# Performance work log

Measured on AMD Instinct MI355X. Metric: run time of the kernel, lower is better.

## Reference

```python
import jax, jax.numpy as jnp
import numpy as np

BEAM_SIZE = 16


def setup_inputs() -> dict:
    key = jax.random.key(0)
    ks = jax.random.split(key, 9)
    B, N, S, A, Ai, E = 4, 48, 32, 16, 8, 512
    unaries = jax.random.normal(ks[0], (B, N, S), jnp.float32)
    behaviors = jax.random.normal(ks[1], (B, N, S, A), jnp.float32)
    interactions = jax.random.normal(ks[2], (B, N, N, S, S, Ai), jnp.float32)
    masks = jnp.ones((B, N), jnp.bool_)
    behavior_masks = jax.random.bernoulli(ks[3], 0.5, (S, A))
    interaction_masks = jax.random.bernoulli(ks[4], 0.5, (S, S, Ai))
    binary_edges = jax.random.randint(ks[5], (B, E, 2), 0, N, jnp.int32)
    binary_masks = jnp.ones((B, E), jnp.bool_)
    targets = jax.random.randint(ks[6], (B, N), 0, S, jnp.int32)
    weight_param_unary = jax.random.uniform(ks[7], (S,), jnp.float32)
    weight_param_binary = jax.random.uniform(ks[8], (S, S), jnp.float32)
    return dict(unaries=unaries, behaviors=behaviors, interactions=interactions,
                weight_param_unary=weight_param_unary, weight_param_binary=weight_param_binary,
                masks=masks, behavior_masks=behavior_masks, interaction_masks=interaction_masks,
                binary_edges=binary_edges, binary_masks=binary_masks, targets=targets)


def _forward(unaries, behaviors, interactions, weight_param_unary, weight_param_binary,
             masks, behavior_masks, interaction_masks, binary_edges, binary_masks, targets):
    sg = jax.lax.stop_gradient  # mirrors torch.no_grad blocks
    B, N, S = unaries.shape
    E = binary_edges.shape[1]
    K = min(BEAM_SIZE, S)
    dt = unaries.dtype

    m = masks[..., None].astype(dt)                                  # (B,N,1)
    masked_unaries = sg(unaries * m)                                 # no_grad
    bmask = behavior_masks.astype(dt)                                # (S,A)
    acnt = bmask.sum(-1)
    acnt = jnp.where(acnt == 0, jnp.ones((), dt), acnt)              # (S,)
    behaviors_unaries = sg(((behaviors * bmask).sum(-1) / acnt) * m) # (B,N,S), no_grad

    weighted_unaries = masked_unaries + weight_param_unary * behaviors_unaries

    # --- beam selection (targets forced to beam slot 0 via +inf scatter) ---
    bi = jnp.arange(B)[:, None]
    ni = jnp.arange(N)[None, :]
    _u = weighted_unaries.at[bi, ni, targets].set(jnp.inf)
    beam_targets = jax.lax.top_k(sg(_u), K)[1]                       # (B,N,K) int
    beam_unary = jnp.take_along_axis(weighted_unaries, beam_targets, axis=2)  # (B,N,K)

    # --- binary potentials: masked mean over interaction actions ---
    imask = interaction_masks.astype(dt)                             # (S,S,Ai)
    icnt = imask.sum(-1)
    icnt = jnp.where(icnt == 0, jnp.ones((), dt), icnt)              # (S,S)
    masked_inter = (interactions * imask).sum(-1) / icnt             # (B,N,N,S,S)

    eb = jnp.arange(B)[:, None]
    sel = masked_inter[eb, binary_edges[..., 0], binary_edges[..., 1]]  # (B,E,S,S)
    bt1 = beam_targets[eb, binary_edges[..., 0]]                     # (B,E,K)
    bt2 = beam_targets[eb, binary_edges[..., 1]]                     # (B,E,K)
    bin_phis_init = sg(sel[jnp.arange(B)[:, None, None, None],
                           jnp.arange(E)[None, :, None, None],
                           bt1[:, :, :, None], bt2[:, :, None, :]])  # (B,E,K,K), no_grad
    bin_phis = bin_phis_init * weight_param_binary[bt1[:, :, :, None], bt2[:, :, None, :]]

    # --- piecewise pseudo-likelihood loss ---
    norm_unary = jax.nn.log_softmax(beam_unary, axis=-1)
    gold_unary = jnp.where(masks, norm_unary[:, :, 0], jnp.zeros((), dt))
    pll = gold_unary.sum(-1)                                         # (B,)
    norm_bin = jax.nn.log_softmax(bin_phis.reshape(B, E, K * K), axis=-1).reshape(B, E, K, K)
    gold_bin = jnp.where(binary_masks, norm_bin[:, :, 0, 0], jnp.zeros((), dt))
    pll = pll + gold_bin.sum(-1)
    nll = -(pll / masks.sum(-1).astype(dt)).mean()
    return nll


def reference(unaries, behaviors, interactions, weight_param_unary, weight_param_binary,
              masks, behavior_masks, interaction_masks, binary_edges, binary_masks, targets):
    return _forward(unaries, behaviors, interactions, weight_param_unary, weight_param_binary,
                    masks, behavior_masks, interaction_masks, binary_edges, binary_masks, targets)
```

## Files before the change

kernel.cpp:

```cpp
#include <hip/hip_runtime.h>
#include <hip/hip_bf16.h>
#include <math.h>

#define BB 4
#define NN 48
#define SS 32
#define AA 16
#define AI 8
#define EE 512
#define KK 16
#define NNODE (BB * NN)
#define NEDGE (BB * EE)

#define WS_NG    0
#define WS_EG    1024

__device__ __forceinline__ bool read_mask(const void* p, int idx, int flag) {
    if (flag == 1) return ((const unsigned char*)p)[idx] != 0;
    if (flag == 2) return ((const float*)p)[idx] != 0.0f;
    return ((const int*)p)[idx] != 0;
}

__device__ __forceinline__ int detect_flag(const void* bmask, int lane) {
    unsigned int wrd = ((const unsigned int*)bmask)[lane & 31];
    bool anyF = __any(wrd == 0x3F800000u);
    bool anyG = __any(wrd > 1u);
    return anyF ? 2 : (anyG ? 1 : 0);
}

__device__ __forceinline__ void node_beam(
    int node, int lane, int flag,
    const float* __restrict__ unaries, const float* __restrict__ behaviors,
    const void* masks, const int* __restrict__ targets,
    const float* __restrict__ wpu, const void* bmask,
    int* beam16, float* gold_out)
{
    float m = read_mask(masks, node, flag) ? 1.f : 0.f;
    int tgt = targets[node];

    float val = -INFINITY, key = -INFINITY;
    if (lane < SS) {
        int s = lane;
        float u = unaries[node * SS + s];

        const float4* bp4 = (const float4*)(behaviors + ((size_t)node * SS + s) * AA);
        float4 b0 = bp4[0], b1 = bp4[1], b2 = bp4[2], b3 = bp4[3];
        float bv[16] = {b0.x,b0.y,b0.z,b0.w, b1.x,b1.y,b1.z,b1.w,
                        b2.x,b2.y,b2.z,b2.w, b3.x,b3.y,b3.z,b3.w};

        float bmv[16];
        if (flag == 1) {
            uint4 v = *(const uint4*)((const unsigned char*)bmask + s * 16);
            unsigned int w4[4] = {v.x, v.y, v.z, v.w};
            #pragma unroll
            for (int k = 0; k < 16; ++k)
                bmv[k] = ((w4[k >> 2] >> ((k & 3) * 8)) & 255u) ? 1.f : 0.f;
        } else if (flag == 0) {
            const uint4* ip = (const uint4*)((const int*)bmask + s * 16);
            #pragma unroll
            for (int r = 0; r < 4; ++r) {
                uint4 v = ip[r];
                bmv[r*4+0] = v.x ? 1.f : 0.f; bmv[r*4+1] = v.y ? 1.f : 0.f;
                bmv[r*4+2] = v.z ? 1.f : 0.f; bmv[r*4+3] = v.w ? 1.f : 0.f;
            }
        } else {
            const float4* fp = (const float4*)((const float*)bmask + s * 16);
            #pragma unroll
            for (int r = 0; r < 4; ++r) {
                float4 v = fp[r];
                bmv[r*4+0] = v.x != 0.f ? 1.f : 0.f; bmv[r*4+1] = v.y != 0.f ? 1.f : 0.f;
                bmv[r*4+2] = v.z != 0.f ? 1.f : 0.f; bmv[r*4+3] = v.w != 0.f ? 1.f : 0.f;
            }
        }

        float cnt = 0.f, raw = 0.f;
        #pragma unroll
        for (int k = 0; k < 16; ++k) { cnt += bmv[k]; raw += bmv[k] * bv[k]; }
        if (cnt == 0.f) cnt = 1.f;
        val = m * (u + wpu[s] * (raw / cnt));
        key = (s == tgt) ? INFINITY : val;
    }

    int rank = 0;
    #pragma unroll
    for (int t = 0; t < SS; ++t) {
        float kt = __shfl(key, t, 64);
        rank += (kt > key) || (kt == key && t < lane);
    }
    bool sel = (lane < SS) && (rank < KK);

    if (beam16) {
        bool sel_nt = sel && (lane != tgt);
        unsigned long long bal = __ballot(sel_nt);
        if (sel) {
            int slot = (lane == tgt) ? 0
                       : 1 + __popcll(bal & ((1ull << lane) - 1ull));
            beam16[slot] = lane;
        }
    }

    if (gold_out) {
        float mv = sel ? val : -INFINITY;
        #pragma unroll
        for (int off = 32; off >= 1; off >>= 1)
            mv = fmaxf(mv, __shfl_xor(mv, off, 64));
        float se = sel ? expf(val - mv) : 0.f;
        #pragma unroll
        for (int off = 32; off >= 1; off >>= 1)
            se += __shfl_xor(se, off, 64);
        float vt = __shfl(val, tgt, 64);
        if (lane == 0)
            *gold_out = (m > 0.f) ? (vt - mv - logf(se)) : 0.f;
    }
}

__global__ __launch_bounds__(256) void main_kernel(
    const float* __restrict__ unaries,
    const float* __restrict__ behaviors,
    const float* __restrict__ interactions,
    const float* __restrict__ wpu,
    const float* __restrict__ wpb,
    const void* masks, const void* bmask, const void* imask,
    const int* __restrict__ edges, const void* binmask,
    const int* __restrict__ targets,
    float* __restrict__ node_gold,
    float* __restrict__ edge_gold)
{
    int be = blockIdx.x;
    int b = be >> 9;
    int tid = threadIdx.x;
    int wid = tid >> 6, lane = tid & 63;
    int flag = detect_flag(bmask, lane);

    int2 e2 = ((const int2*)edges)[be];
    int n1 = e2.x, n2 = e2.y;

    __shared__ int beamA[KK], beamB[KK];

    bool active = (wid < 2) || (wid == 2 && be < NNODE);
    if (active) {
        int node = (wid == 0) ? (b * NN + n1)
                 : (wid == 1) ? (b * NN + n2) : be;
        int* bptr = (wid == 0) ? beamA : (wid == 1) ? beamB : nullptr;
        float* gptr = (wid == 2) ? &node_gold[be] : nullptr;
        node_beam(node, lane, flag, unaries, behaviors, masks, targets,
                  wpu, bmask, bptr, gptr);
    }
    __syncthreads();

    int i = tid >> 4, j = tid & 15;
    int s1 = beamA[i], s2 = beamB[j];
    int p = s1 * SS + s2;

    size_t base = (((size_t)(b * NN + n1) * NN + n2) * (SS * SS) + p) * AI;
    float4 x0 = *(const float4*)(interactions + base);
    float4 x1 = *(const float4*)(interactions + base + 4);
    float xv[8] = {x0.x,x0.y,x0.z,x0.w, x1.x,x1.y,x1.z,x1.w};

    float imv[8];
    if (flag == 1) {
        uint2 v = *(const uint2*)((const unsigned char*)imask + p * 8);
        unsigned int w2[2] = {v.x, v.y};
        #pragma unroll
        for (int k = 0; k < 8; ++k)
            imv[k] = ((w2[k >> 2] >> ((k & 3) * 8)) & 255u) ? 1.f : 0.f;
    } else if (flag == 0) {
        const uint4* ip = (const uint4*)((const int*)imask + p * 8);
        uint4 v0 = ip[0], v1 = ip[1];
        imv[0]=v0.x?1.f:0.f; imv[1]=v0.y?1.f:0.f; imv[2]=v0.z?1.f:0.f; imv[3]=v0.w?1.f:0.f;
        imv[4]=v1.x?1.f:0.f; imv[5]=v1.y?1.f:0.f; imv[6]=v1.z?1.f:0.f; imv[7]=v1.w?1.f:0.f;
    } else {
        const float4* fp = (const float4*)((const float*)imask + p * 8);
        float4 v0 = fp[0], v1 = fp[1];
        imv[0]=v0.x!=0.f?1.f:0.f; imv[1]=v0.y!=0.f?1.f:0.f; imv[2]=v0.z!=0.f?1.f:0.f; imv[3]=v0.w!=0.f?1.f:0.f;
        imv[4]=v1.x!=0.f?1.f:0.f; imv[5]=v1.y!=0.f?1.f:0.f; imv[6]=v1.z!=0.f?1.f:0.f; imv[7]=v1.w!=0.f?1.f:0.f;
    }
    float cnt = 0.f, raw = 0.f;
    #pragma unroll
    for (int k = 0; k < 8; ++k) { cnt += imv[k]; raw += imv[k] * xv[k]; }
    if (cnt == 0.f) cnt = 1.f;
    float phi = wpb[p] * (raw / cnt);

    float mw = phi;
    #pragma unroll
    for (int off = 32; off >= 1; off >>= 1)
        mw = fmaxf(mw, __shfl_xor(mw, off, 64));
    float ew = expf(phi - mw);
    #pragma unroll
    for (int off = 32; off >= 1; off >>= 1)
        ew += __shfl_xor(ew, off, 64);

    __shared__ float2 sred[4];
    if (lane == 0) sred[wid] = make_float2(mw, ew);
    __syncthreads();

    if (tid == 0) {
        float2 p0 = sred[0], p1 = sred[1], p2 = sred[2], p3 = sred[3];
        float M = fmaxf(fmaxf(p0.x, p1.x), fmaxf(p2.x, p3.x));
        float S = p0.y * expf(p0.x - M) + p1.y * expf(p1.x - M)
                + p2.y * expf(p2.x - M) + p3.y * expf(p3.x - M);
        float gold = phi - M - logf(S);
        bool bm = read_mask(binmask, be, flag);
        edge_gold[be] = bm ? gold : 0.f;
    }
}

__global__ __launch_bounds__(256) void final_kernel(
    const void* masks, const void* bmask,
    const float* __restrict__ node_gold,
    const float* __restrict__ edge_gold,
    float* __restrict__ out)
{
    int tid = threadIdx.x;
    int b = tid >> 6;
    int lane = tid & 63;
    int flag = detect_flag(bmask, lane);

    float sum = 0.f, cnt = 0.f;
    if (lane < NN) {
        sum += node_gold[b * NN + lane];
        cnt += read_mask(masks, b * NN + lane, flag) ? 1.f : 0.f;
    }
    for (int e = lane; e < EE; e += 64)
        sum += edge_gold[b * EE + e];

    #pragma unroll
    for (int off = 32; off >= 1; off >>= 1) {
        sum += __shfl_xor(sum, off, 64);
        cnt += __shfl_xor(cnt, off, 64);
    }
    __shared__ float sp[4];
    if (lane == 0) sp[b] = sum / cnt;
    __syncthreads();
    if (tid == 0)
        out[0] = -(sp[0] + sp[1] + sp[2] + sp[3]) * (1.f / BB);
}

extern "C" void kernel_launch(void* const* d_in, const int* in_sizes, int n_in,
                              void* d_out, int out_size, void* d_ws, size_t ws_size,
                              hipStream_t stream) {
    const float* unaries      = (const float*)d_in[0];
    const float* behaviors    = (const float*)d_in[1];
    const float* interactions = (const float*)d_in[2];
    const float* wpu          = (const float*)d_in[3];
    const float* wpb          = (const float*)d_in[4];
    const void*  masks        = d_in[5];
    const void*  bmask        = d_in[6];
    const void*  imask        = d_in[7];
    const int*   edges        = (const int*)d_in[8];
    const void*  binmask      = d_in[9];
    const int*   targets      = (const int*)d_in[10];
    float* out = (float*)d_out;

    char* ws = (char*)d_ws;
    float* node_gold = (float*)(ws + WS_NG);
    float* edge_gold = (float*)(ws + WS_EG);

    main_kernel<<<NEDGE, 256, 0, stream>>>(unaries, behaviors, interactions,
                                           wpu, wpb, masks, bmask, imask,
                                           edges, binmask, targets,
                                           node_gold, edge_gold);
    final_kernel<<<1, 256, 0, stream>>>(masks, bmask, node_gold, edge_gold, out);
}
```

Measured before the change: 17.59 us.

## Compute per-wave redundant beams to drop block barrier; split node gold to extra blocks

Every wave now computes both endpoint beams itself, with each 32-lane half handling one node and writing to a per-wave shared slot. This removes the block-wide barrier between beam selection and the interaction pass. Node gold-unary work moves into 48 extra blocks, so edge blocks no longer carry a third divergent wave. The cost is fourfold redundant beam computation per edge block, paid to avoid the __syncthreads stall. The final reduction also reads edge_gold with float4 loads.

```diff
diff --git a/kernel.cpp b/kernel.cpp
--- a/kernel.cpp
+++ b/kernel.cpp
@@ -28,90 +28,48 @@
     return anyF ? 2 : (anyG ? 1 : 0);
 }
 
-__device__ __forceinline__ void node_beam(
-    int node, int lane, int flag,
+__device__ __forceinline__ float weighted_unary(
+    int node, int s, int flag, float m,
     const float* __restrict__ unaries, const float* __restrict__ behaviors,
-    const void* masks, const int* __restrict__ targets,
-    const float* __restrict__ wpu, const void* bmask,
-    int* beam16, float* gold_out)
+    const float* __restrict__ wpu, const void* bmask)
 {
-    float m = read_mask(masks, node, flag) ? 1.f : 0.f;
-    int tgt = targets[node];
-
-    float val = -INFINITY, key = -INFINITY;
-    if (lane < SS) {
-        int s = lane;
-        float u = unaries[node * SS + s];
-
-        const float4* bp4 = (const float4*)(behaviors + ((size_t)node * SS + s) * AA);
-        float4 b0 = bp4[0], b1 = bp4[1], b2 = bp4[2], b3 = bp4[3];
-        float bv[16] = {b0.x,b0.y,b0.z,b0.w, b1.x,b1.y,b1.z,b1.w,
-                        b2.x,b2.y,b2.z,b2.w, b3.x,b3.y,b3.z,b3.w};
-
-        float bmv[16];
-        if (flag == 1) {
-            uint4 v = *(const uint4*)((const unsigned char*)bmask + s * 16);
-            unsigned int w4[4] = {v.x, v.y, v.z, v.w};
-            #pragma unroll
-            for (int k = 0; k < 16; ++k)
-                bmv[k] = ((w4[k >> 2] >> ((k & 3) * 8)) & 255u) ? 1.f : 0.f;
-        } else if (flag == 0) {
-            const uint4* ip = (const uint4*)((const int*)bmask + s * 16);
-            #pragma unroll
-            for (int r = 0; r < 4; ++r) {
-                uint4 v = ip[r];
-                bmv[r*4+0] = v.x ? 1.f : 0.f; bmv[r*4+1] = v.y ? 1.f : 0.f;
-                bmv[r*4+2] = v.z ? 1.f : 0.f; bmv[r*4+3] = v.w ? 1.f : 0.f;
-            }
-        } else {
-            const float4* fp = (const float4*)((const float*)bmask + s * 16);
-            #pragma unroll
-            for (int r = 0; r < 4; ++r) {
-                float4 v = fp[r];
-                bmv[r*4+0] = v.x != 0.f ? 1.f : 0.f; bmv[r*4+1] = v.y != 0.f ? 1.f : 0.f;
-                bmv[r*4+2] = v.z != 0.f ? 1.f : 0.f; bmv[r*4+3] = v.w != 0.f ? 1.f : 0.f;
-            }
-        }
-
-        float cnt = 0.f, raw = 0.f;
-        #pragma unroll
-        for (int k = 0; k < 16; ++k) { cnt += bmv[k]; raw += bmv[k] * bv[k]; }
-        if (cnt == 0.f) cnt = 1.f;
-        val = m * (u + wpu[s] * (raw / cnt));
-        key = (s == tgt) ? INFINITY : val;
-    }
-
-    int rank = 0;
-    #pragma unroll
-    for (int t = 0; t < SS; ++t) {
-        float kt = __shfl(key, t, 64);
-        rank += (kt > key) || (kt == key && t < lane);
-    }
-    bool sel = (lane < SS) && (rank < KK);
-
-    if (beam16) {
-        bool sel_nt = sel && (lane != tgt);
-        unsigned long long bal = __ballot(sel_nt);
-        if (sel) {
-            int slot = (lane == tgt) ? 0
-                       : 1 + __popcll(bal & ((1ull << lane) - 1ull));
-            beam16[slot] = lane;
-        }
-    }
-
-    if (gold_out) {
-        float mv = sel ? val : -INFINITY;
-        #pragma unroll
-        for (int off = 32; off >= 1; off >>= 1)
-            mv = fmaxf(mv, __shfl_xor(mv, off, 64));
-        float se = sel ? expf(val - mv) : 0.f;
-        #pragma unroll
-        for (int off = 32; off >= 1; off >>= 1)
-            se += __shfl_xor(se, off, 64);
-        float vt = __shfl(val, tgt, 64);
-        if (lane == 0)
-            *gold_out = (m > 0.f) ? (vt - mv - logf(se)) : 0.f;
-    }
+    float u = unaries[node * SS + s];
+
+    const float4* bp4 = (const float4*)(behaviors + ((size_t)node * SS + s) * AA);
+    float4 b0 = bp4[0], b1 = bp4[1], b2 = bp4[2], b3 = bp4[3];
+    float bv[16] = {b0.x,b0.y,b0.z,b0.w, b1.x,b1.y,b1.z,b1.w,
+                    b2.x,b2.y,b2.z,b2.w, b3.x,b3.y,b3.z,b3.w};
+
+    float bmv[16];
+    if (flag == 1) {
+        uint4 v = *(const uint4*)((const unsigned char*)bmask + s * 16);
+        unsigned int w4[4] = {v.x, v.y, v.z, v.w};
+        #pragma unroll
+        for (int k = 0; k < 16; ++k)
+            bmv[k] = ((w4[k >> 2] >> ((k & 3) * 8)) & 255u) ? 1.f : 0.f;
+    } else if (flag == 0) {
+        const uint4* ip = (const uint4*)((const int*)bmask + s * 16);
+        #pragma unroll
+        for (int r = 0; r < 4; ++r) {
+            uint4 v = ip[r];
+            bmv[r*4+0] = v.x ? 1.f : 0.f; bmv[r*4+1] = v.y ? 1.f : 0.f;
+            bmv[r*4+2] = v.z ? 1.f : 0.f; bmv[r*4+3] = v.w ? 1.f : 0.f;
+        }
+    } else {
+        const float4* fp = (const float4*)((const float*)bmask + s * 16);
+        #pragma unroll
+        for (int r = 0; r < 4; ++r) {
+            float4 v = fp[r];
+            bmv[r*4+0] = v.x != 0.f ? 1.f : 0.f; bmv[r*4+1] = v.y != 0.f ? 1.f : 0.f;
+            bmv[r*4+2] = v.z != 0.f ? 1.f : 0.f; bmv[r*4+3] = v.w != 0.f ? 1.f : 0.f;
+        }
+    }
+
+    float cnt = 0.f, raw = 0.f;
+    #pragma unroll
+    for (int k = 0; k < 16; ++k) { cnt += bmv[k]; raw += bmv[k] * bv[k]; }
+    if (cnt == 0.f) cnt = 1.f;
+    return m * (u + wpu[s] * (raw / cnt));
 }
 
 __global__ __launch_bounds__(256) void main_kernel(
@@ -126,35 +84,85 @@
     float* __restrict__ node_gold,
     float* __restrict__ edge_gold)
 {
-    int be = blockIdx.x;
-    int b = be >> 9;
     int tid = threadIdx.x;
     int wid = tid >> 6, lane = tid & 63;
     int flag = detect_flag(bmask, lane);
 
+    if (blockIdx.x >= NEDGE) {
+        int node = (blockIdx.x - NEDGE) * 4 + wid;
+        float m = read_mask(masks, node, flag) ? 1.f : 0.f;
+        int tgt = targets[node];
+
+        float val = -INFINITY, key = -INFINITY;
+        if (lane < SS) {
+            val = weighted_unary(node, lane, flag, m, unaries, behaviors, wpu, bmask);
+            key = (lane == tgt) ? INFINITY : val;
+        }
+        int rank = 0;
+        #pragma unroll
+        for (int t = 0; t < SS; ++t) {
+            float kt = __shfl(key, t, 64);
+            rank += (kt > key) || (kt == key && t < lane);
+        }
+        bool sel = (lane < SS) && (rank < KK);
+
+        float mv = sel ? val : -INFINITY;
+        #pragma unroll
+        for (int off = 32; off >= 1; off >>= 1)
+            mv = fmaxf(mv, __shfl_xor(mv, off, 64));
+        float se = sel ? expf(val - mv) : 0.f;
+        #pragma unroll
+        for (int off = 32; off >= 1; off >>= 1)
+            se += __shfl_xor(se, off, 64);
+        float vt = __shfl(val, tgt, 64);
+        if (lane == 0)
+            node_gold[node] = (m > 0.f) ? (vt - mv - logf(se)) : 0.f;
+        return;
+    }
+
+    int be = blockIdx.x;
+    int b = be >> 9;
+    int half = lane >> 5;
+    int s = lane & 31;
+
     int2 e2 = ((const int2*)edges)[be];
     int n1 = e2.x, n2 = e2.y;
-
-    __shared__ int beamA[KK], beamB[KK];
-
-    bool active = (wid < 2) || (wid == 2 && be < NNODE);
-    if (active) {
-        int node = (wid == 0) ? (b * NN + n1)
-                 : (wid == 1) ? (b * NN + n2) : be;
-        int* bptr = (wid == 0) ? beamA : (wid == 1) ? beamB : nullptr;
-        float* gptr = (wid == 2) ? &node_gold[be] : nullptr;
-        node_beam(node, lane, flag, unaries, behaviors, masks, targets,
-                  wpu, bmask, bptr, gptr);
-    }
-    __syncthreads();
-
-    int i = tid >> 4, j = tid & 15;
-    int s1 = beamA[i], s2 = beamB[j];
+    int node = b * NN + (half ? n2 : n1);
+
+    __shared__ int beamW[4][2 * KK];
+    __shared__ float2 sred[4];
+
+    float m = read_mask(masks, node, flag) ? 1.f : 0.f;
+    int tgt = targets[node];
+    float val = weighted_unary(node, s, flag, m, unaries, behaviors, wpu, bmask);
+    float key = (s == tgt) ? INFINITY : val;
+
+    int base = half << 5;
+    int rank = 0;
+    #pragma unroll
+    for (int t = 0; t < SS; ++t) {
+        float kt = __shfl(key, base + t, 64);
+        rank += (kt > key) || (kt == key && t < s);
+    }
+    bool sel = rank < KK;
+
+    bool sel_nt = sel && (s != tgt);
+    unsigned long long bal = __ballot(sel_nt);
+    unsigned int hb = (unsigned int)(bal >> (half << 5));
+    if (sel) {
+        int slot = (s == tgt) ? 0 : 1 + __popc(hb & ((1u << s) - 1u));
+        beamW[wid][(half << 4) + slot] = s;
+    }
+
+    int i = (wid << 2) + (lane >> 4);
+    int j = lane & 15;
+    int s1 = beamW[wid][i];
+    int s2 = beamW[wid][16 + j];
     int p = s1 * SS + s2;
 
-    size_t base = (((size_t)(b * NN + n1) * NN + n2) * (SS * SS) + p) * AI;
-    float4 x0 = *(const float4*)(interactions + base);
-    float4 x1 = *(const float4*)(interactions + base + 4);
+    size_t gbase = (((size_t)(b * NN + n1) * NN + n2) * (SS * SS) + p) * AI;
+    float4 x0 = *(const float4*)(interactions + gbase);
+    float4 x1 = *(const float4*)(interactions + gbase + 4);
     float xv[8] = {x0.x,x0.y,x0.z,x0.w, x1.x,x1.y,x1.z,x1.w};
 
     float imv[8];
@@ -190,7 +198,6 @@
     for (int off = 32; off >= 1; off >>= 1)
         ew += __shfl_xor(ew, off, 64);
 
-    __shared__ float2 sred[4];
     if (lane == 0) sred[wid] = make_float2(mw, ew);
     __syncthreads();
 
@@ -221,8 +228,12 @@
         sum += node_gold[b * NN + lane];
         cnt += read_mask(masks, b * NN + lane, flag) ? 1.f : 0.f;
     }
-    for (int e = lane; e < EE; e += 64)
-        sum += edge_gold[b * EE + e];
+    const float4* eg4 = (const float4*)(edge_gold + b * EE);
+    #pragma unroll
+    for (int k = 0; k < 2; ++k) {
+        float4 v = eg4[(lane << 1) + k];
+        sum += v.x + v.y + v.z + v.w;
+    }
 
     #pragma unroll
     for (int off = 32; off >= 1; off >>= 1) {
@@ -256,9 +267,9 @@
     float* node_gold = (float*)(ws + WS_NG);
     float* edge_gold = (float*)(ws + WS_EG);
 
-    main_kernel<<<NEDGE, 256, 0, stream>>>(unaries, behaviors, interactions,
-                                           wpu, wpb, masks, bmask, imask,
-                                           edges, binmask, targets,
-                                           node_gold, edge_gold);
+    main_kernel<<<NEDGE + 48, 256, 0, stream>>>(unaries, behaviors, interactions,
+                                                wpu, wpb, masks, bmask, imask,
+                                                edges, binmask, targets,
+                                                node_gold, edge_gold);
     final_kernel<<<1, 256, 0, stream>>>(masks, bmask, node_gold, edge_gold, out);
 }
```

Result: no change. 17.65 us (+0.3%).
